# Performance work log

Measured on AMD Instinct MI355X. Metric: run time of the kernel, lower is better.

Reference implementation:

```python
import jax, jax.numpy as jnp
import numpy as np

N = 100000   # nodes
E = 1600000  # edges
F_IN = 32    # num_features
H = 16       # hidden_size (hardcoded as conv2 input in source)
C = 10       # num_classes
K = 2        # kernel_size (dim=1)


def setup_inputs() -> dict:
    key = jax.random.key(0)
    ks = jax.random.split(key, 9)
    x = jax.random.normal(ks[0], (N, F_IN), dtype=jnp.float32)
    edge_index = jax.random.randint(ks[1], (2, E), 0, N, dtype=jnp.int64)
    edge_attr = jax.random.uniform(ks[2], (E, 1), dtype=jnp.float32)
    s1 = 1.0 / np.sqrt(F_IN)
    s2 = 1.0 / np.sqrt(H)
    W1 = jax.random.normal(ks[3], (K, F_IN, H), dtype=jnp.float32) * s1
    root1 = jax.random.normal(ks[4], (F_IN, H), dtype=jnp.float32) * s1
    b1 = jnp.zeros((H,), dtype=jnp.float32)
    W2 = jax.random.normal(ks[5], (K, H, C), dtype=jnp.float32) * s2
    root2 = jax.random.normal(ks[6], (H, C), dtype=jnp.float32) * s2
    b2 = jnp.zeros((C,), dtype=jnp.float32)
    return {"x": x, "edge_index": edge_index, "edge_attr": edge_attr,
            "W1": W1, "root1": root1, "b1": b1,
            "W2": W2, "root2": root2, "b2": b2}


def spline_conv(x, edge_index, edge_attr, W, root, bias, num_nodes):
    # Open B-spline, degree 1: hat-function basis over K knots.
    k = W.shape[0]
    src, dst = edge_index[0], edge_index[1]
    v = edge_attr[:, 0] * (k - 1)                                   # [E]
    grid = jnp.arange(k, dtype=v.dtype)
    basis = jnp.maximum(0.0, 1.0 - jnp.abs(v[:, None] - grid[None, :]))  # [E,K]
    xe = x[src]                                                      # [E,in] gather
    msg = jnp.einsum('ei,kio,ek->eo', xe, W, basis)                  # per-edge message
    agg = jax.ops.segment_sum(msg, dst, num_segments=num_nodes)      # scatter-add
    deg = jax.ops.segment_sum(jnp.ones((msg.shape[0],), x.dtype), dst,
                              num_segments=num_nodes)
    agg = agg / jnp.maximum(deg, 1.0)[:, None]                       # mean aggregation
    return agg + x @ root + bias


def reference(x, edge_index, edge_attr, W1, root1, b1, W2, root2, b2):
    # Inference mode: F.dropout(training=False) is identity.
    h = jax.nn.elu(spline_conv(x, edge_index, edge_attr, W1, root1, b1, N))
    out = spline_conv(h, edge_index, edge_attr, W2, root2, b2, N)
    return jax.nn.log_softmax(out, axis=1)
```

## Files before the change

### kernel.cpp

```cpp
#include <hip/hip_runtime.h>
#include <math.h>

#define N_NODES 100000
#define E_EDGES 1600000
#define F_IN 32
#define HID 16
#define NC 10
#define SRC_BITS 17
#define SRC_MASK ((1u << SRC_BITS) - 1u)
#define VQ_SCALE 32767.0f
#define CBITS 8
#define BUCKET_N 256
#define NCB ((N_NODES + BUCKET_N - 1) / BUCKET_N)
#define BLK_E 4096
#define NBLK ((E_EDGES + BLK_E - 1) / BLK_E)
#define L1_BLOCKS ((N_NODES + 511) / 512)
#define CAP 6144

__device__ __forceinline__ unsigned int bf16pair(float lo, float hi) {
    unsigned int ulo = __float_as_uint(lo), uhi = __float_as_uint(hi);
    ulo += 0x7fffu + ((ulo >> 16) & 1u);
    uhi += 0x7fffu + ((uhi >> 16) & 1u);
    return (ulo >> 16) | (uhi & 0xffff0000u);
}

__device__ __forceinline__ float lerp_pair(unsigned int pair, float v) {
    float a = __uint_as_float(pair << 16);
    float b = __uint_as_float(pair & 0xffff0000u);
    return fmaf(v, b - a, a);
}

__global__ __launch_bounds__(512) void fused_l1bucket(
    const float* __restrict__ x, const float* __restrict__ W1,
    const float* __restrict__ root1, const float* __restrict__ b1,
    const int* __restrict__ ei, const float* __restrict__ ea,
    unsigned int* __restrict__ y, float* __restrict__ r1,
    int* __restrict__ gcur, int2* __restrict__ ebuf)
{
    if (blockIdx.x >= L1_BLOCKS) {
        __shared__ int h[NCB], base[NCB], cur[NCB];
        __shared__ int wsum[8], woff[8];
        __shared__ unsigned int  pay_lds[BLK_E];
        __shared__ unsigned char dl_lds[BLK_E];
        __shared__ int           gid_lds[BLK_E];
        int t = threadIdx.x;
        int b = blockIdx.x - L1_BLOCKS;
        for (int i = t; i < NCB; i += 512) { h[i] = 0; cur[i] = 0; }
        __syncthreads();

        const int* dstp = ei + E_EDGES;
        int e0 = b * BLK_E + t * 8;
        int4 dA, dB, sA, sB;
        float4 aA, aB;
        bool fullA = (e0 + 3 < E_EDGES), fullB = (e0 + 7 < E_EDGES);
        if (fullA) {
            dA = *(const int4*)(dstp + e0);
            sA = *(const int4*)(ei + e0);
            aA = *(const float4*)(ea + e0);
            atomicAdd(&h[dA.x >> CBITS], 1);
            atomicAdd(&h[dA.y >> CBITS], 1);
            atomicAdd(&h[dA.z >> CBITS], 1);
            atomicAdd(&h[dA.w >> CBITS], 1);
        }
        if (fullB) {
            dB = *(const int4*)(dstp + e0 + 4);
            sB = *(const int4*)(ei + e0 + 4);
            aB = *(const float4*)(ea + e0 + 4);
            atomicAdd(&h[dB.x >> CBITS], 1);
            atomicAdd(&h[dB.y >> CBITS], 1);
            atomicAdd(&h[dB.z >> CBITS], 1);
            atomicAdd(&h[dB.w >> CBITS], 1);
        }
        if (!fullA || !fullB) {
            int lo = fullA ? e0 + 4 : e0;
            for (int e = lo; e < E_EDGES && e < e0 + 8; e++)
                atomicAdd(&h[dstp[e] >> CBITS], 1);
        }
        __syncthreads();

        for (int s = t; s < NCB; s += 512)
            base[s] = (h[s] > 0) ? atomicAdd(&gcur[s], h[s]) : 0;
        __syncthreads();

        int w = t >> 6, l = t & 63;
        int v = (t < NCB) ? h[t] : 0;
        int incl = v;
        #pragma unroll
        for (int off = 1; off < 64; off <<= 1) {
            int u = __shfl_up(incl, off, 64);
            if (l >= off) incl += u;
        }
        if (l == 63) wsum[w] = incl;
        __syncthreads();
        if (t == 0) {
            int a = 0;
            #pragma unroll
            for (int i = 0; i < 8; i++) { woff[i] = a; a += wsum[i]; }
        }
        __syncthreads();
        if (t < NCB) h[t] = woff[w] + incl - v;
        __syncthreads();

        #define STAGE(dv, sv, av) do {                                          \
            int s_ = (dv) >> CBITS;                                             \
            int idx_ = atomicAdd(&cur[s_], 1);                                  \
            int p_ = h[s_] + idx_;                                              \
            int g_ = base[s_] + idx_;                                           \
            gid_lds[p_] = (g_ < CAP) ? (s_ * CAP + g_) : -1;                    \
            unsigned int vq_ = (unsigned int)((av) * VQ_SCALE + 0.5f);          \
            pay_lds[p_] = (vq_ << SRC_BITS) | (unsigned int)(sv);               \
            dl_lds[p_] = (unsigned char)((dv) & (BUCKET_N - 1));                \
        } while (0)

        if (fullA) {
            STAGE(dA.x, sA.x, aA.x);
            STAGE(dA.y, sA.y, aA.y);
            STAGE(dA.z, sA.z, aA.z);
            STAGE(dA.w, sA.w, aA.w);
        }
        if (fullB) {
            STAGE(dB.x, sB.x, aB.x);
            STAGE(dB.y, sB.y, aB.y);
            STAGE(dB.z, sB.z, aB.z);
            STAGE(dB.w, sB.w, aB.w);
        }
        if (!fullA || !fullB) {
            int lo = fullA ? e0 + 4 : e0;
            for (int e = lo; e < E_EDGES && e < e0 + 8; e++)
                STAGE(dstp[e], ei[e], ea[e]);
        }
        #undef STAGE
        __syncthreads();

        int nE = min(BLK_E, E_EDGES - b * BLK_E);
        for (int p = t; p < nE; p += 512) {
            int g = gid_lds[p];
            if (g >= 0)
                ebuf[g] = make_int2((int)dl_lds[p], (int)pay_lds[p]);
        }
        return;
    }
    __shared__ float sW0[F_IN * HID], sW1[F_IN * HID], sR[F_IN * HID], sB[HID];
    for (int i = threadIdx.x; i < F_IN * HID; i += 512) {
        sW0[i] = W1[i];
        sW1[i] = W1[F_IN * HID + i];
        sR[i]  = root1[i];
    }
    if (threadIdx.x < HID) sB[threadIdx.x] = b1[threadIdx.x];
    __syncthreads();

    int n = blockIdx.x * 512 + threadIdx.x;
    if (n >= N_NODES) return;

    float xr[F_IN];
    const float4* xp = (const float4*)(x + (size_t)n * F_IN);
    #pragma unroll
    for (int i = 0; i < F_IN / 4; i++) {
        float4 t4 = xp[i];
        xr[i*4+0] = t4.x; xr[i*4+1] = t4.y; xr[i*4+2] = t4.z; xr[i*4+3] = t4.w;
    }

    float a0[HID], a1[HID], ar[HID];
    #pragma unroll
    for (int o = 0; o < HID; o++) { a0[o] = 0.f; a1[o] = 0.f; ar[o] = sB[o]; }
    for (int i = 0; i < F_IN; i++) {
        float xi = xr[i];
        #pragma unroll
        for (int o = 0; o < HID; o++) {
            a0[o] += xi * sW0[i * HID + o];
            a1[o] += xi * sW1[i * HID + o];
            ar[o] += xi * sR[i * HID + o];
        }
    }
    unsigned int* py = y + (size_t)n * 16;
    float* pr = r1 + (size_t)n * HID;
    #pragma unroll
    for (int o = 0; o < HID; o++) {
        py[o] = bf16pair(a0[o], a1[o]);
        pr[o] = ar[o];
    }
}

__global__ __launch_bounds__(1024) void k_bsort(
    const int2* __restrict__ ebuf, const int* __restrict__ gcur,
    unsigned int* __restrict__ es, int* __restrict__ start)
{
    __shared__ int hist[BUCKET_N];
    __shared__ int cursor[BUCKET_N];
    __shared__ int pre[NCB];
    __shared__ int wsum[16], woff[16];
    __shared__ int wsum2[4], woff2[4];
    __shared__ unsigned char dl_lds[CAP];
    __shared__ unsigned int  pay_lds[CAP];
    __shared__ unsigned int  es_lds[CAP];
    int t = threadIdx.x;
    int b = blockIdx.x;
    int w = t >> 6, l = t & 63;

    int v = (t < NCB) ? min(gcur[t], CAP) : 0;
    int incl = v;
    #pragma unroll
    for (int off = 1; off < 64; off <<= 1) {
        int u = __shfl_up(incl, off, 64);
        if (l >= off) incl += u;
    }
    if (l == 63) wsum[w] = incl;
    if (t < BUCKET_N) { hist[t] = 0; cursor[t] = 0; }
    __syncthreads();
    if (t == 0) {
        int a = 0;
        #pragma unroll
        for (int i = 0; i < 16; i++) { woff[i] = a; a += wsum[i]; }
    }
    __syncthreads();
    if (t < NCB) pre[t] = woff[w] + incl - v;
    __syncthreads();

    int fill = min(gcur[b], CAP);
    int obase = pre[b];
    const int2* win = ebuf + (size_t)b * CAP;

    for (int j = t; j < fill; j += 1024) {
        int2 p = win[j];
        dl_lds[j]  = (unsigned char)p.x;
        pay_lds[j] = (unsigned int)p.y;
    }
    __syncthreads();

    for (int j = t; j < fill; j += 1024)
        atomicAdd(&hist[dl_lds[j]], 1);
    __syncthreads();

    int c = (t < BUCKET_N) ? hist[t] : 0;
    int incl2 = c;
    #pragma unroll
    for (int off = 1; off < 64; off <<= 1) {
        int u = __shfl_up(incl2, off, 64);
        if (l >= off) incl2 += u;
    }
    if (w < 4 && l == 63) wsum2[w] = incl2;
    __syncthreads();
    if (t == 0) {
        int acc = 0;
        #pragma unroll
        for (int i = 0; i < 4; i++) { woff2[i] = acc; acc += wsum2[i]; }
    }
    __syncthreads();
    if (t < BUCKET_N) {
        int excl = woff2[w] + incl2 - c;
        hist[t] = excl;
        int node = (b << CBITS) + t;
        if (node < N_NODES) start[node] = obase + excl;
    }
    if (b == 0 && t == 0) start[N_NODES] = E_EDGES;
    __syncthreads();

    for (int j = t; j < fill; j += 1024) {
        int d = dl_lds[j];
        int off = atomicAdd(&cursor[d], 1);
        es_lds[hist[d] + off] = pay_lds[j];
    }
    __syncthreads();
    for (int j = t; j < fill; j += 1024)
        es[obase + j] = es_lds[j];
}

__global__ __launch_bounds__(256) void k_agg1(
    const unsigned int* __restrict__ es, const int* __restrict__ start,
    const unsigned int* __restrict__ y, const float* __restrict__ r1,
    const float* __restrict__ W2, const float* __restrict__ root2,
    const float* __restrict__ b2,
    unsigned int* __restrict__ z, float* __restrict__ r2)
{
    __shared__ float sW0[HID * NC], sW1[HID * NC], sRt[HID * NC], sB2[NC];
    int t = threadIdx.x;
    if (t < HID * NC) { sW0[t] = W2[t]; sW1[t] = W2[HID * NC + t]; sRt[t] = root2[t]; }
    if (t >= HID * NC && t < HID * NC + NC) sB2[t - HID * NC] = b2[t - HID * NC];
    __syncthreads();

    int idx = blockIdx.x * 256 + t;
    int n = idx >> 2, l = idx & 3;
    if (n >= N_NODES) return;
    int j0 = start[n], j1 = start[n + 1];
    const uint4* yrow = (const uint4*)y;
    float acc[4] = {0.f, 0.f, 0.f, 0.f};
    int j = j0;
    for (; j + 3 < j1; j += 4) {
        unsigned int p0 = es[j], p1 = es[j+1], p2 = es[j+2], p3 = es[j+3];
        uint4 q0 = yrow[(size_t)(p0 & SRC_MASK) * 4 + l];
        uint4 q1 = yrow[(size_t)(p1 & SRC_MASK) * 4 + l];
        uint4 q2 = yrow[(size_t)(p2 & SRC_MASK) * 4 + l];
        uint4 q3 = yrow[(size_t)(p3 & SRC_MASK) * 4 + l];
        float v0 = (float)(p0 >> SRC_BITS) * (1.0f / VQ_SCALE);
        float v1 = (float)(p1 >> SRC_BITS) * (1.0f / VQ_SCALE);
        float v2 = (float)(p2 >> SRC_BITS) * (1.0f / VQ_SCALE);
        float v3 = (float)(p3 >> SRC_BITS) * (1.0f / VQ_SCALE);
        acc[0] += lerp_pair(q0.x, v0); acc[1] += lerp_pair(q0.y, v0);
        acc[2] += lerp_pair(q0.z, v0); acc[3] += lerp_pair(q0.w, v0);
        acc[0] += lerp_pair(q1.x, v1); acc[1] += lerp_pair(q1.y, v1);
        acc[2] += lerp_pair(q1.z, v1); acc[3] += lerp_pair(q1.w, v1);
        acc[0] += lerp_pair(q2.x, v2); acc[1] += lerp_pair(q2.y, v2);
        acc[2] += lerp_pair(q2.z, v2); acc[3] += lerp_pair(q2.w, v2);
        acc[0] += lerp_pair(q3.x, v3); acc[1] += lerp_pair(q3.y, v3);
        acc[2] += lerp_pair(q3.z, v3); acc[3] += lerp_pair(q3.w, v3);
    }
    for (; j < j1; j++) {
        unsigned int p = es[j];
        uint4 q = yrow[(size_t)(p & SRC_MASK) * 4 + l];
        float v = (float)(p >> SRC_BITS) * (1.0f / VQ_SCALE);
        acc[0] += lerp_pair(q.x, v); acc[1] += lerp_pair(q.y, v);
        acc[2] += lerp_pair(q.z, v); acc[3] += lerp_pair(q.w, v);
    }
    float inv = 1.0f / fmaxf((float)(j1 - j0), 1.0f);
    float4 rr = *(const float4*)(r1 + (size_t)n * HID + l * 4);
    float hv[4];
    hv[0] = acc[0] * inv + rr.x;
    hv[1] = acc[1] * inv + rr.y;
    hv[2] = acc[2] * inv + rr.z;
    hv[3] = acc[3] * inv + rr.w;
    #pragma unroll
    for (int e = 0; e < 4; e++) hv[e] = hv[e] > 0.0f ? hv[e] : expm1f(hv[e]);

    int cbase = l * 4;
    float a0[4] = {0.f, 0.f, 0.f, 0.f}, a1[4] = {0.f, 0.f, 0.f, 0.f}, ar[4];
    #pragma unroll
    for (int e = 0; e < 4; e++) { int c = cbase + e; ar[e] = (c < NC) ? sB2[c] : 0.f; }
    #pragma unroll
    for (int s = 0; s < 4; s++) {
        #pragma unroll
        for (int e2 = 0; e2 < 4; e2++) {
            float hi = __shfl(hv[e2], s, 4);
            int i = s * 4 + e2;
            #pragma unroll
            for (int e = 0; e < 4; e++) {
                int c = cbase + e;
                if (c < NC) {
                    a0[e] += hi * sW0[i * NC + c];
                    a1[e] += hi * sW1[i * NC + c];
                    ar[e] += hi * sRt[i * NC + c];
                }
            }
        }
    }
    uint4 zo;
    zo.x = (cbase + 0 < NC) ? bf16pair(a0[0], a1[0]) : 0u;
    zo.y = (cbase + 1 < NC) ? bf16pair(a0[1], a1[1]) : 0u;
    zo.z = (cbase + 2 < NC) ? bf16pair(a0[2], a1[2]) : 0u;
    zo.w = (cbase + 3 < NC) ? bf16pair(a0[3], a1[3]) : 0u;
    ((uint4*)z)[(size_t)n * 4 + l] = zo;
    #pragma unroll
    for (int e = 0; e < 4; e++) {
        int c = cbase + e;
        if (c < NC) r2[(size_t)n * NC + c] = ar[e];
    }
}

__global__ __launch_bounds__(256) void k_agg2(
    const unsigned int* __restrict__ es, const int* __restrict__ start,
    const unsigned int* __restrict__ z,
    const float* __restrict__ r2, float* __restrict__ out)
{
    int idx = blockIdx.x * 256 + threadIdx.x;
    int n = idx >> 2, l = idx & 3;
    if (n >= N_NODES) return;
    int j0 = start[n], j1 = start[n + 1];
    const uint4* zrow = (const uint4*)z;
    float acc[4] = {0.f, 0.f, 0.f, 0.f};
    int j = j0;
    for (; j + 3 < j1; j += 4) {
        unsigned int p0 = es[j], p1 = es[j+1], p2 = es[j+2], p3 = es[j+3];
        uint4 q0 = zrow[(size_t)(p0 & SRC_MASK) * 4 + l];
        uint4 q1 = zrow[(size_t)(p1 & SRC_MASK) * 4 + l];
        uint4 q2 = zrow[(size_t)(p2 & SRC_MASK) * 4 + l];
        uint4 q3 = zrow[(size_t)(p3 & SRC_MASK) * 4 + l];
        float v0 = (float)(p0 >> SRC_BITS) * (1.0f / VQ_SCALE);
        float v1 = (float)(p1 >> SRC_BITS) * (1.0f / VQ_SCALE);
        float v2 = (float)(p2 >> SRC_BITS) * (1.0f / VQ_SCALE);
        float v3 = (float)(p3 >> SRC_BITS) * (1.0f / VQ_SCALE);
        acc[0] += lerp_pair(q0.x, v0); acc[1] += lerp_pair(q0.y, v0);
        acc[2] += lerp_pair(q0.z, v0); acc[3] += lerp_pair(q0.w, v0);
        acc[0] += lerp_pair(q1.x, v1); acc[1] += lerp_pair(q1.y, v1);
        acc[2] += lerp_pair(q1.z, v1); acc[3] += lerp_pair(q1.w, v1);
        acc[0] += lerp_pair(q2.x, v2); acc[1] += lerp_pair(q2.y, v2);
        acc[2] += lerp_pair(q2.z, v2); acc[3] += lerp_pair(q2.w, v2);
        acc[0] += lerp_pair(q3.x, v3); acc[1] += lerp_pair(q3.y, v3);
        acc[2] += lerp_pair(q3.z, v3); acc[3] += lerp_pair(q3.w, v3);
    }
    for (; j < j1; j++) {
        unsigned int p = es[j];
        uint4 q = zrow[(size_t)(p & SRC_MASK) * 4 + l];
        float v = (float)(p >> SRC_BITS) * (1.0f / VQ_SCALE);
        acc[0] += lerp_pair(q.x, v); acc[1] += lerp_pair(q.y, v);
        acc[2] += lerp_pair(q.z, v); acc[3] += lerp_pair(q.w, v);
    }
    float inv = 1.0f / fmaxf((float)(j1 - j0), 1.0f);
    int cbase = l * 4;
    float val[4];
    #pragma unroll
    for (int e = 0; e < 4; e++) {
        int c = cbase + e;
        val[e] = (c < NC) ? acc[e] * inv + r2[(size_t)n * NC + c] : -INFINITY;
    }
    float mx = fmaxf(fmaxf(val[0], val[1]), fmaxf(val[2], val[3]));
    mx = fmaxf(mx, __shfl_xor(mx, 1, 4));
    mx = fmaxf(mx, __shfl_xor(mx, 2, 4));
    float ssum = 0.f;
    #pragma unroll
    for (int e = 0; e < 4; e++) {
        int c = cbase + e;
        if (c < NC) ssum += expf(val[e] - mx);
    }
    ssum += __shfl_xor(ssum, 1, 4);
    ssum += __shfl_xor(ssum, 2, 4);
    float lse = logf(ssum);
    #pragma unroll
    for (int e = 0; e < 4; e++) {
        int c = cbase + e;
        if (c < NC) out[(size_t)n * NC + c] = val[e] - mx - lse;
    }
}

extern "C" void kernel_launch(void* const* d_in, const int* in_sizes, int n_in,
                              void* d_out, int out_size, void* d_ws, size_t ws_size,
                              hipStream_t stream) {
    const float* x     = (const float*)d_in[0];
    const int*   ei    = (const int*)d_in[1];
    const float* ea    = (const float*)d_in[2];
    const float* W1    = (const float*)d_in[3];
    const float* root1 = (const float*)d_in[4];
    const float* b1    = (const float*)d_in[5];
    const float* W2    = (const float*)d_in[6];
    const float* root2 = (const float*)d_in[7];
    const float* b2    = (const float*)d_in[8];
    float* out = (float*)d_out;

    char* wsb = (char*)d_ws;
    int2*         ebuf   = (int2*)wsb;
    unsigned int* es     = (unsigned int*)(wsb + (size_t)NCB * CAP * 8);
    unsigned int* y      = es + (size_t)E_EDGES;
    float*        r1     = (float*)(y + (size_t)N_NODES * 16);
    unsigned int* z      = (unsigned int*)(r1 + (size_t)N_NODES * HID);
    float*        r2     = (float*)(z + (size_t)N_NODES * 16);
    int*          start  = (int*)(r2 + (size_t)N_NODES * NC);
    int*          gcur   = start + N_NODES + 1;

    int aggGrid = (N_NODES * 4 + 255) / 256;

    hipMemsetAsync(gcur, 0, (size_t)NCB * sizeof(int), stream);
    fused_l1bucket<<<L1_BLOCKS + NBLK, 512, 0, stream>>>(x, W1, root1, b1, ei, ea,
                                                         y, r1, gcur, ebuf);
    k_bsort<<<NCB, 1024, 0, stream>>>(ebuf, gcur, es, start);
    k_agg1 <<<aggGrid, 256, 0, stream>>>(es, start, y, r1, W2, root2, b2, z, r2);
    k_agg2 <<<aggGrid, 256, 0, stream>>>(es, start, z, r2, out);
}
```

Before: 167.6 us.

## Fuse layer-1 aggregation into bucket sort kernel using LDS-resident edge lists

Merges the first aggregation kernel into the bucket-sort kernel. Each 1024-thread block handles its 256 destination nodes with 4 lanes per node, reading the sorted edge payloads straight from LDS and taking degrees from the per-bucket cursors. This removes one kernel launch and the global re-read of the sorted edge array and start offsets. The cost is that layer-1 aggregation now runs at the sort kernel's occupancy, with 1024 threads per block and large LDS use, which may hide gather latency less well than the old 256-thread launch.

```diff
diff --git a/kernel.cpp b/kernel.cpp
--- a/kernel.cpp
+++ b/kernel.cpp
@@ -181,9 +181,13 @@
     }
 }
 
-__global__ __launch_bounds__(1024) void k_bsort(
+__global__ __launch_bounds__(1024) void k_bsort_agg1(
     const int2* __restrict__ ebuf, const int* __restrict__ gcur,
-    unsigned int* __restrict__ es, int* __restrict__ start)
+    unsigned int* __restrict__ es, int* __restrict__ start,
+    const unsigned int* __restrict__ y, const float* __restrict__ r1,
+    const float* __restrict__ W2, const float* __restrict__ root2,
+    const float* __restrict__ b2,
+    unsigned int* __restrict__ z, float* __restrict__ r2)
 {
     __shared__ int hist[BUCKET_N];
     __shared__ int cursor[BUCKET_N];
@@ -193,9 +197,13 @@
     __shared__ unsigned char dl_lds[CAP];
     __shared__ unsigned int  pay_lds[CAP];
     __shared__ unsigned int  es_lds[CAP];
+    __shared__ float sW0[HID * NC], sW1[HID * NC], sRt[HID * NC], sB2[NC];
     int t = threadIdx.x;
     int b = blockIdx.x;
     int w = t >> 6, l = t & 63;
+
+    if (t < HID * NC) { sW0[t] = W2[t]; sW1[t] = W2[HID * NC + t]; sRt[t] = root2[t]; }
+    if (t >= HID * NC && t < HID * NC + NC) sB2[t - HID * NC] = b2[t - HID * NC];
 
     int v = (t < NCB) ? min(gcur[t], CAP) : 0;
     int incl = v;
@@ -261,36 +269,25 @@
         es_lds[hist[d] + off] = pay_lds[j];
     }
     __syncthreads();
+
     for (int j = t; j < fill; j += 1024)
         es[obase + j] = es_lds[j];
-}
-
-__global__ __launch_bounds__(256) void k_agg1(
-    const unsigned int* __restrict__ es, const int* __restrict__ start,
-    const unsigned int* __restrict__ y, const float* __restrict__ r1,
-    const float* __restrict__ W2, const float* __restrict__ root2,
-    const float* __restrict__ b2,
-    unsigned int* __restrict__ z, float* __restrict__ r2)
-{
-    __shared__ float sW0[HID * NC], sW1[HID * NC], sRt[HID * NC], sB2[NC];
-    int t = threadIdx.x;
-    if (t < HID * NC) { sW0[t] = W2[t]; sW1[t] = W2[HID * NC + t]; sRt[t] = root2[t]; }
-    if (t >= HID * NC && t < HID * NC + NC) sB2[t - HID * NC] = b2[t - HID * NC];
-    __syncthreads();
-
-    int idx = blockIdx.x * 256 + t;
-    int n = idx >> 2, l = idx & 3;
-    if (n >= N_NODES) return;
-    int j0 = start[n], j1 = start[n + 1];
+
+    int n = t >> 2, l4 = t & 3;
+    int node = (b << CBITS) + n;
+    if (node >= N_NODES) return;
+    int jj0 = hist[n];
+    int deg = cursor[n];
+    int jj1 = jj0 + deg;
     const uint4* yrow = (const uint4*)y;
     float acc[4] = {0.f, 0.f, 0.f, 0.f};
-    int j = j0;
-    for (; j + 3 < j1; j += 4) {
-        unsigned int p0 = es[j], p1 = es[j+1], p2 = es[j+2], p3 = es[j+3];
-        uint4 q0 = yrow[(size_t)(p0 & SRC_MASK) * 4 + l];
-        uint4 q1 = yrow[(size_t)(p1 & SRC_MASK) * 4 + l];
-        uint4 q2 = yrow[(size_t)(p2 & SRC_MASK) * 4 + l];
-        uint4 q3 = yrow[(size_t)(p3 & SRC_MASK) * 4 + l];
+    int j = jj0;
+    for (; j + 3 < jj1; j += 4) {
+        unsigned int p0 = es_lds[j], p1 = es_lds[j+1], p2 = es_lds[j+2], p3 = es_lds[j+3];
+        uint4 q0 = yrow[(size_t)(p0 & SRC_MASK) * 4 + l4];
+        uint4 q1 = yrow[(size_t)(p1 & SRC_MASK) * 4 + l4];
+        uint4 q2 = yrow[(size_t)(p2 & SRC_MASK) * 4 + l4];
+        uint4 q3 = yrow[(size_t)(p3 & SRC_MASK) * 4 + l4];
         float v0 = (float)(p0 >> SRC_BITS) * (1.0f / VQ_SCALE);
         float v1 = (float)(p1 >> SRC_BITS) * (1.0f / VQ_SCALE);
         float v2 = (float)(p2 >> SRC_BITS) * (1.0f / VQ_SCALE);
@@ -304,15 +301,15 @@
         acc[0] += lerp_pair(q3.x, v3); acc[1] += lerp_pair(q3.y, v3);
         acc[2] += lerp_pair(q3.z, v3); acc[3] += lerp_pair(q3.w, v3);
     }
-    for (; j < j1; j++) {
-        unsigned int p = es[j];
-        uint4 q = yrow[(size_t)(p & SRC_MASK) * 4 + l];
-        float v = (float)(p >> SRC_BITS) * (1.0f / VQ_SCALE);
-        acc[0] += lerp_pair(q.x, v); acc[1] += lerp_pair(q.y, v);
-        acc[2] += lerp_pair(q.z, v); acc[3] += lerp_pair(q.w, v);
-    }
-    float inv = 1.0f / fmaxf((float)(j1 - j0), 1.0f);
-    float4 rr = *(const float4*)(r1 + (size_t)n * HID + l * 4);
+    for (; j < jj1; j++) {
+        unsigned int p = es_lds[j];
+        uint4 q = yrow[(size_t)(p & SRC_MASK) * 4 + l4];
+        float vv = (float)(p >> SRC_BITS) * (1.0f / VQ_SCALE);
+        acc[0] += lerp_pair(q.x, vv); acc[1] += lerp_pair(q.y, vv);
+        acc[2] += lerp_pair(q.z, vv); acc[3] += lerp_pair(q.w, vv);
+    }
+    float inv = 1.0f / fmaxf((float)deg, 1.0f);
+    float4 rr = *(const float4*)(r1 + (size_t)node * HID + l4 * 4);
     float hv[4];
     hv[0] = acc[0] * inv + rr.x;
     hv[1] = acc[1] * inv + rr.y;
@@ -321,10 +318,10 @@
     #pragma unroll
     for (int e = 0; e < 4; e++) hv[e] = hv[e] > 0.0f ? hv[e] : expm1f(hv[e]);
 
-    int cbase = l * 4;
+    int cbase = l4 * 4;
     float a0[4] = {0.f, 0.f, 0.f, 0.f}, a1[4] = {0.f, 0.f, 0.f, 0.f}, ar[4];
     #pragma unroll
-    for (int e = 0; e < 4; e++) { int c = cbase + e; ar[e] = (c < NC) ? sB2[c] : 0.f; }
+    for (int e = 0; e < 4; e++) { int cc = cbase + e; ar[e] = (cc < NC) ? sB2[cc] : 0.f; }
     #pragma unroll
     for (int s = 0; s < 4; s++) {
         #pragma unroll
@@ -333,11 +330,11 @@
             int i = s * 4 + e2;
             #pragma unroll
             for (int e = 0; e < 4; e++) {
-                int c = cbase + e;
-                if (c < NC) {
-                    a0[e] += hi * sW0[i * NC + c];
-                    a1[e] += hi * sW1[i * NC + c];
-                    ar[e] += hi * sRt[i * NC + c];
+                int cc = cbase + e;
+                if (cc < NC) {
+                    a0[e] += hi * sW0[i * NC + cc];
+                    a1[e] += hi * sW1[i * NC + cc];
+                    ar[e] += hi * sRt[i * NC + cc];
                 }
             }
         }
@@ -347,11 +344,11 @@
     zo.y = (cbase + 1 < NC) ? bf16pair(a0[1], a1[1]) : 0u;
     zo.z = (cbase + 2 < NC) ? bf16pair(a0[2], a1[2]) : 0u;
     zo.w = (cbase + 3 < NC) ? bf16pair(a0[3], a1[3]) : 0u;
-    ((uint4*)z)[(size_t)n * 4 + l] = zo;
+    ((uint4*)z)[(size_t)node * 4 + l4] = zo;
     #pragma unroll
     for (int e = 0; e < 4; e++) {
-        int c = cbase + e;
-        if (c < NC) r2[(size_t)n * NC + c] = ar[e];
+        int cc = cbase + e;
+        if (cc < NC) r2[(size_t)node * NC + cc] = ar[e];
     }
 }
 
@@ -449,7 +446,7 @@
     hipMemsetAsync(gcur, 0, (size_t)NCB * sizeof(int), stream);
     fused_l1bucket<<<L1_BLOCKS + NBLK, 512, 0, stream>>>(x, W1, root1, b1, ei, ea,
                                                          y, r1, gcur, ebuf);
-    k_bsort<<<NCB, 1024, 0, stream>>>(ebuf, gcur, es, start);
-    k_agg1 <<<aggGrid, 256, 0, stream>>>(es, start, y, r1, W2, root2, b2, z, r2);
+    k_bsort_agg1<<<NCB, 1024, 0, stream>>>(ebuf, gcur, es, start,
+                                           y, r1, W2, root2, b2, z, r2);
     k_agg2 <<<aggGrid, 256, 0, stream>>>(es, start, z, r2, out);
 }
```

New measurement: 161.5 us (median of 2 runs). -3.6%, faster.
